# Optimization experiments

Measured on AMD Instinct MI355X. Metric: run time of the kernel, lower is better.

Reference implementation:

```python
import jax, jax.numpy as jnp
import numpy as np


def setup_inputs() -> dict:
    key = jax.random.key(0)
    ks = jax.random.split(key, 5)
    B, S, H = 64, 1024, 1024
    scale = 1.0 / np.sqrt(H)
    return {
        "decoder_hidden": jax.random.normal(ks[0], (B, H), jnp.float32),
        "encoder_outputs": jax.random.normal(ks[1], (B, S, H), jnp.float32),
        "W1": jax.random.normal(ks[2], (H, H), jnp.float32) * scale,
        "W2": jax.random.normal(ks[3], (H, H), jnp.float32) * scale,
        "v": jax.random.normal(ks[4], (H,), jnp.float32) * scale,
    }


def reference(decoder_hidden, encoder_outputs, W1, W2, v):
    # W1 @ decoder_hidden: [B, H] computed once, broadcast over src_len
    dh_proj = jnp.einsum("bh,oh->bo", decoder_hidden, W1)          # [B, H]
    enc_proj = jnp.einsum("bsh,oh->bso", encoder_outputs, W2)      # [B, S, H]
    energy = jnp.tanh(dh_proj[:, None, :] + enc_proj)              # [B, S, H]
    scores = jnp.einsum("bsh,h->bs", energy, v)                    # [B, S]
    attention_weights = jax.nn.softmax(scores, axis=-1)            # [B, S]
    context = jnp.einsum("bs,bsh->bh", attention_weights, encoder_outputs)
    return (context, attention_weights)
```

## Files before the change

kernel.cpp:

```cpp
#include <hip/hip_runtime.h>
#include <hip/hip_bf16.h>
#include <cmath>

#define Hdim 1024
#define Bdim 64
#define Sdim 1024

typedef __attribute__((ext_vector_type(4))) float f32x4;
typedef __attribute__((ext_vector_type(8))) short s16x8;
typedef __attribute__((ext_vector_type(4))) unsigned int u32x4;

static __device__ __forceinline__ unsigned short f2bf(float f) {
  unsigned int u = __builtin_bit_cast(unsigned int, f);
  unsigned int r = (u + 0x7fffu + ((u >> 16) & 1u)) >> 16;
  return (unsigned short)r;
}

static __device__ __forceinline__ float bf2f(unsigned short u) {
  return __builtin_bit_cast(float, (unsigned int)u << 16);
}

#define TANH_C 2.885390081777927f


static __device__ __forceinline__ void stage_rows64(const float* __restrict__ src,
                                                    unsigned short* As, int tid) {
  #pragma unroll 4
  for (int i = 0; i < 32; ++i) {
    int c = tid + i * 256;
    int row = c >> 7;
    int k8 = (c & 127) << 3;
    const float4* p = reinterpret_cast<const float4*>(src + row * Hdim + k8);
    float4 a = p[0];
    float4 b = p[1];
    union { unsigned short us[8]; u32x4 v; } pk;
    pk.us[0] = f2bf(a.x); pk.us[1] = f2bf(a.y); pk.us[2] = f2bf(a.z); pk.us[3] = f2bf(a.w);
    pk.us[4] = f2bf(b.x); pk.us[5] = f2bf(b.y); pk.us[6] = f2bf(b.z); pk.us[7] = f2bf(b.w);
    int idx = row * Hdim + (k8 ^ ((row & 7) << 3));
    *reinterpret_cast<u32x4*>(&As[idx]) = pk.v;
  }
}

static __device__ __forceinline__ s16x8 lda_full(const unsigned short* As, int row, int k) {
  int idx = row * Hdim + (k ^ ((row & 7) << 3));
  return *reinterpret_cast<const s16x8*>(&As[idx]);
}

static __device__ __forceinline__ s16x8 ldb_g(const unsigned short* __restrict__ Wb,
                                              const float* __restrict__ Wf,
                                              int use_bf, int o, int k) {
  if (use_bf) {
    return *reinterpret_cast<const s16x8*>(&Wb[o * Hdim + k]);
  } else {
    const float4* p = reinterpret_cast<const float4*>(Wf + o * Hdim + k);
    float4 a = p[0];
    float4 b = p[1];
    union { unsigned short us[8]; s16x8 v; } pk;
    pk.us[0] = f2bf(a.x); pk.us[1] = f2bf(a.y); pk.us[2] = f2bf(a.z); pk.us[3] = f2bf(a.w);
    pk.us[4] = f2bf(b.x); pk.us[5] = f2bf(b.y); pk.us[6] = f2bf(b.z); pk.us[7] = f2bf(b.w);
    return pk.v;
  }
}

__global__ void cast_bf16_kernel(const float* __restrict__ src,
                                 unsigned short* __restrict__ dst) {
  int i = blockIdx.x * 256 + threadIdx.x;
  const float4* p = reinterpret_cast<const float4*>(src) + i * 2;
  float4 a = p[0];
  float4 b = p[1];
  union { unsigned short us[8]; u32x4 v; } pk;
  pk.us[0] = f2bf(a.x); pk.us[1] = f2bf(a.y); pk.us[2] = f2bf(a.z); pk.us[3] = f2bf(a.w);
  pk.us[4] = f2bf(b.x); pk.us[5] = f2bf(b.y); pk.us[6] = f2bf(b.z); pk.us[7] = f2bf(b.w);
  *reinterpret_cast<u32x4*>(dst + i * 8) = pk.v;
}

__global__ __launch_bounds__(256, 1) void proj_kernel(
    const float* __restrict__ dh, const float* __restrict__ W1f,
    const unsigned short* __restrict__ W1b, float* __restrict__ out, int use_bf) {
  __shared__ unsigned short As[64 * Hdim];
  int tid = threadIdx.x;
  stage_rows64(dh, As, tid);
  __syncthreads();
  int w = tid >> 6, lane = tid & 63;
  int lo = lane & 15, hi = lane >> 4;
  int o = blockIdx.x * 16 + lo;
  f32x4 acc = {0.f, 0.f, 0.f, 0.f};
  for (int k0 = 0; k0 < Hdim; k0 += 32) {
    int k = k0 + hi * 8;
    s16x8 bfrag = ldb_g(W1b, W1f, use_bf, o, k);
    s16x8 afrag = lda_full(As, w * 16 + lo, k);
    acc = __builtin_amdgcn_mfma_f32_16x16x32_bf16(afrag, bfrag, acc, 0, 0, 0);
  }
  #pragma unroll
  for (int r = 0; r < 4; ++r)
    out[(w * 16 + hi * 4 + r) * Hdim + o] = acc[r];
}

#define SBM 128
#define SBN 128
#define SBK 64

__global__ __launch_bounds__(256, 3) void score_mfma_kernel(
    const unsigned short* __restrict__ encb,
    const unsigned short* __restrict__ W2b,
    const float* __restrict__ dhp, const float* __restrict__ v,
    float* __restrict__ scores) {
  __shared__ unsigned short As[2][SBM * SBK];
  __shared__ unsigned short Bs[2][SBN * SBK];
  __shared__ float ssum[SBM];
  int tid = threadIdx.x;
  int bid = blockIdx.x;
  int swz = (bid & 7) * 512 + (bid >> 3);
  int mp = swz >> 3;
  int np = swz & 7;
  int row0 = mp * SBM;
  int b = row0 >> 10;
  int w = tid >> 6, lane = tid & 63;
  int wr = w >> 1, wc = w & 1;
  int lo = lane & 15, hi = lane >> 4;

  if (tid < SBM) ssum[tid] = 0.f;

  const unsigned short* gA[4];
  const unsigned short* gB[4];
  #pragma unroll
  for (int i = 0; i < 4; ++i) {
    int d = i * 256 + tid;
    int row = d >> 3, c = d & 7;
    int gc = c ^ (row & 7);
    gA[i] = encb + (size_t)(row0 + row) * Hdim + gc * 8;
    gB[i] = W2b + (size_t)(np * SBN + row) * Hdim + gc * 8;
  }

  auto STAGE = [&](int buf) {
    #pragma unroll
    for (int i = 0; i < 4; ++i) {
      int dwv = i * 256 + w * 64;
      __builtin_amdgcn_global_load_lds(
          (const __attribute__((address_space(1))) unsigned int*)gA[i],
          (__attribute__((address_space(3))) unsigned int*)(&As[buf][dwv * 8]), 16, 0, 0);
      __builtin_amdgcn_global_load_lds(
          (const __attribute__((address_space(1))) unsigned int*)gB[i],
          (__attribute__((address_space(3))) unsigned int*)(&Bs[buf][dwv * 8]), 16, 0, 0);
      gA[i] += SBK;
      gB[i] += SBK;
    }
  };

  f32x4 acc[4][4] = {};

  STAGE(0);
  asm volatile("s_waitcnt vmcnt(0)" ::: "memory");
  __syncthreads();

  int cur = 0;
  for (int t = 0; t < 16; ++t) {
    if (t < 15) STAGE(cur ^ 1);

    const char* Ab = (const char*)As[cur];
    const char* Bb = (const char*)Bs[cur];
    #pragma unroll
    for (int ks = 0; ks < 2; ++ks) {
      int kb = (ks * 32 + hi * 8) * 2;
      s16x8 af[4], bf[4];
      #pragma unroll
      for (int m = 0; m < 4; ++m) {
        int row = wr * 64 + m * 16 + lo;
        af[m] = *reinterpret_cast<const s16x8*>(Ab + row * (SBK * 2) + (kb ^ ((row & 7) << 4)));
      }
      #pragma unroll
      for (int n = 0; n < 4; ++n) {
        int row = wc * 64 + n * 16 + lo;
        bf[n] = *reinterpret_cast<const s16x8*>(Bb + row * (SBK * 2) + (kb ^ ((row & 7) << 4)));
      }
      #pragma unroll
      for (int m = 0; m < 4; ++m)
        #pragma unroll
        for (int n = 0; n < 4; ++n)
          acc[m][n] = __builtin_amdgcn_mfma_f32_16x16x32_bf16(af[m], bf[n], acc[m][n], 0, 0, 0);
    }
    asm volatile("s_waitcnt vmcnt(0)" ::: "memory");
    __syncthreads();
    cur ^= 1;
  }

  float psum[4][4] = {};
  #pragma unroll
  for (int n = 0; n < 4; ++n) {
    int o = np * SBN + wc * 64 + n * 16 + lo;
    float dv = dhp[b * Hdim + o];
    float vv = v[o];
    float vv2 = 2.f * vv;
    #pragma unroll
    for (int m = 0; m < 4; ++m)
      #pragma unroll
      for (int r = 0; r < 4; ++r) {
        float x = acc[m][n][r] + dv;
        float e2 = __builtin_amdgcn_exp2f(x * TANH_C);
        float rc = __builtin_amdgcn_rcpf(1.f + e2);
        psum[m][r] += vv - vv2 * rc;
      }
  }
  #pragma unroll
  for (int mask = 1; mask < 16; mask <<= 1)
    #pragma unroll
    for (int m = 0; m < 4; ++m)
      #pragma unroll
      for (int r = 0; r < 4; ++r)
        psum[m][r] += __shfl_xor(psum[m][r], mask, 64);
  if (lo == 0) {
    #pragma unroll
    for (int m = 0; m < 4; ++m)
      #pragma unroll
      for (int r = 0; r < 4; ++r)
        atomicAdd(&ssum[wr * 64 + m * 16 + hi * 4 + r], psum[m][r]);
  }
  __syncthreads();
  if (tid < SBM) atomicAdd(&scores[row0 + tid], ssum[tid]);
}

#define BKt 64

__global__ __launch_bounds__(256, 3) void score_kernel(
    const float* __restrict__ enc, const float* __restrict__ W2f,
    const unsigned short* __restrict__ W2b, const float* __restrict__ dhp,
    const float* __restrict__ v, float* __restrict__ scores, int use_bf) {
  __shared__ unsigned short As[64 * BKt];
  int tid = threadIdx.x;
  int bid = blockIdx.x;
  int f = (bid & 7) * 512 + (bid >> 3);
  int rg = f >> 2;
  int oc = f & 3;
  int row0 = rg * 64;
  int b = row0 >> 10;
  int w = tid >> 6, lane = tid & 63;
  int lo = lane & 15, hi = lane >> 4;
  int n0 = oc * 256 + w * 64;

  const unsigned short* pB[4];
  const float* pBf[4];
  #pragma unroll
  for (int n = 0; n < 4; ++n) {
    int o = n0 + n * 16 + lo;
    pB[n]  = W2b + (size_t)o * Hdim + hi * 8;
    pBf[n] = W2f + (size_t)o * Hdim + hi * 8;
  }

  f32x4 acc[4][4] = {};

  for (int t = 0; t < 16; ++t) {
    int k0 = t * BKt;
    __syncthreads();
    #pragma unroll
    for (int cc = 0; cc < 2; ++cc) {
      int c = tid + cc * 256;
      int row = c >> 3;
      int j = c & 7;
      const float4* p = reinterpret_cast<const float4*>(
          enc + (size_t)(row0 + row) * Hdim + k0 + j * 8);
      float4 a = p[0];
      float4 bb = p[1];
      union { unsigned short us[8]; u32x4 v4; } pk;
      pk.us[0] = f2bf(a.x);  pk.us[1] = f2bf(a.y);  pk.us[2] = f2bf(a.z);  pk.us[3] = f2bf(a.w);
      pk.us[4] = f2bf(bb.x); pk.us[5] = f2bf(bb.y); pk.us[6] = f2bf(bb.z); pk.us[7] = f2bf(bb.w);
      int idx = row * BKt + ((j * 8) ^ ((row & 7) << 3));
      *reinterpret_cast<u32x4*>(&As[idx]) = pk.v4;
    }
    __syncthreads();

    #pragma unroll
    for (int ks = 0; ks < 2; ++ks) {
      s16x8 bfrag[4];
      #pragma unroll
      for (int n = 0; n < 4; ++n) {
        if (use_bf) {
          bfrag[n] = *reinterpret_cast<const s16x8*>(pB[n] + ks * 32);
        } else {
          const float4* p = reinterpret_cast<const float4*>(pBf[n] + ks * 32);
          float4 a = p[0];
          float4 bb = p[1];
          union { unsigned short us[8]; s16x8 v4; } pk;
          pk.us[0] = f2bf(a.x);  pk.us[1] = f2bf(a.y);  pk.us[2] = f2bf(a.z);  pk.us[3] = f2bf(a.w);
          pk.us[4] = f2bf(bb.x); pk.us[5] = f2bf(bb.y); pk.us[6] = f2bf(bb.z); pk.us[7] = f2bf(bb.w);
          bfrag[n] = pk.v4;
        }
      }
      #pragma unroll
      for (int m = 0; m < 4; ++m) {
        int kk = ks * 32 + hi * 8;
        s16x8 afrag = *reinterpret_cast<const s16x8*>(
            &As[(m * 16 + lo) * BKt + (kk ^ ((lo & 7) << 3))]);
        #pragma unroll
        for (int n = 0; n < 4; ++n)
          acc[m][n] = __builtin_amdgcn_mfma_f32_16x16x32_bf16(afrag, bfrag[n], acc[m][n], 0, 0, 0);
      }
    }
    #pragma unroll
    for (int n = 0; n < 4; ++n) { pB[n] += BKt; pBf[n] += BKt; }
  }

  float psum[4][4] = {};
  #pragma unroll
  for (int n = 0; n < 4; ++n) {
    int o = n0 + n * 16 + lo;
    float dv = dhp[b * Hdim + o];
    float vv = v[o];
    float vv2 = 2.f * vv;
    #pragma unroll
    for (int m = 0; m < 4; ++m)
      #pragma unroll
      for (int r = 0; r < 4; ++r) {
        float x = acc[m][n][r] + dv;
        float e2 = __builtin_amdgcn_exp2f(x * TANH_C);
        float rc = __builtin_amdgcn_rcpf(1.f + e2);
        psum[m][r] += vv - vv2 * rc;
      }
  }
  #pragma unroll
  for (int mask = 1; mask < 16; mask <<= 1)
    #pragma unroll
    for (int m = 0; m < 4; ++m)
      #pragma unroll
      for (int r = 0; r < 4; ++r)
        psum[m][r] += __shfl_xor(psum[m][r], mask, 64);
  if (lo == 0) {
    #pragma unroll
    for (int m = 0; m < 4; ++m)
      #pragma unroll
      for (int r = 0; r < 4; ++r)
        atomicAdd(&scores[row0 + m * 16 + hi * 4 + r], psum[m][r]);
  }
}

__global__ __launch_bounds__(256, 1) void softmax_kernel(float* __restrict__ attn) {
  __shared__ float redm[4];
  __shared__ float reds[4];
  int b = blockIdx.x, tid = threadIdx.x;
  float4 x = *reinterpret_cast<float4*>(attn + b * Sdim + tid * 4);
  float m = fmaxf(fmaxf(x.x, x.y), fmaxf(x.z, x.w));
  #pragma unroll
  for (int mask = 1; mask < 64; mask <<= 1) m = fmaxf(m, __shfl_xor(m, mask, 64));
  if ((tid & 63) == 0) redm[tid >> 6] = m;
  __syncthreads();
  m = fmaxf(fmaxf(redm[0], redm[1]), fmaxf(redm[2], redm[3]));
  float4 e;
  e.x = expf(x.x - m); e.y = expf(x.y - m); e.z = expf(x.z - m); e.w = expf(x.w - m);
  float s = e.x + e.y + e.z + e.w;
  #pragma unroll
  for (int mask = 1; mask < 64; mask <<= 1) s += __shfl_xor(s, mask, 64);
  if ((tid & 63) == 0) reds[tid >> 6] = s;
  __syncthreads();
  s = reds[0] + reds[1] + reds[2] + reds[3];
  float inv = 1.f / s;
  e.x *= inv; e.y *= inv; e.z *= inv; e.w *= inv;
  *reinterpret_cast<float4*>(attn + b * Sdim + tid * 4) = e;
}

__global__ __launch_bounds__(256, 1) void context_bf_kernel(
    const unsigned short* __restrict__ encb, const float* __restrict__ attn,
    float* __restrict__ ctx) {
  int b = blockIdx.x >> 4;
  int chunk = blockIdx.x & 15;
  int tid = threadIdx.x;
  int h0 = tid * 4;
  const unsigned short* ebase = encb + ((size_t)(b * Sdim + chunk * 64)) * Hdim + h0;
  const float* abase = attn + b * Sdim + chunk * 64;
  float4 acc = {0.f, 0.f, 0.f, 0.f};
  #pragma unroll 4
  for (int s = 0; s < 64; ++s) {
    float wgt = abase[s];
    ushort4 ev = *reinterpret_cast<const ushort4*>(ebase + (size_t)s * Hdim);
    acc.x += wgt * bf2f(ev.x);
    acc.y += wgt * bf2f(ev.y);
    acc.z += wgt * bf2f(ev.z);
    acc.w += wgt * bf2f(ev.w);
  }
  float* c = ctx + b * Hdim + h0;
  atomicAdd(c + 0, acc.x);
  atomicAdd(c + 1, acc.y);
  atomicAdd(c + 2, acc.z);
  atomicAdd(c + 3, acc.w);
}

__global__ __launch_bounds__(256, 1) void context_kernel(
    const float* __restrict__ enc, const float* __restrict__ attn,
    float* __restrict__ ctx) {
  int b = blockIdx.x >> 3;
  int chunk = blockIdx.x & 7;
  int tid = threadIdx.x;
  int h0 = tid * 4;
  const float* ebase = enc + ((size_t)(b * Sdim + chunk * 128)) * Hdim + h0;
  const float* abase = attn + b * Sdim + chunk * 128;
  float4 acc = {0.f, 0.f, 0.f, 0.f};
  #pragma unroll 4
  for (int s = 0; s < 128; ++s) {
    float wgt = abase[s];
    float4 ev = *reinterpret_cast<const float4*>(ebase + (size_t)s * Hdim);
    acc.x += wgt * ev.x; acc.y += wgt * ev.y; acc.z += wgt * ev.z; acc.w += wgt * ev.w;
  }
  float* c = ctx + b * Hdim + h0;
  atomicAdd(c + 0, acc.x);
  atomicAdd(c + 1, acc.y);
  atomicAdd(c + 2, acc.z);
  atomicAdd(c + 3, acc.w);
}

extern "C" void kernel_launch(void* const* d_in, const int* in_sizes, int n_in,
                              void* d_out, int out_size, void* d_ws, size_t ws_size,
                              hipStream_t stream) {
  const float* dh  = (const float*)d_in[0];
  const float* enc = (const float*)d_in[1];
  const float* W1  = (const float*)d_in[2];
  const float* W2  = (const float*)d_in[3];
  const float* v   = (const float*)d_in[4];
  float* out_ctx  = (float*)d_out;
  float* out_attn = out_ctx + Bdim * Hdim;

  int use_bf = (ws_size >= 4ull * 1024 * 1024) ? 1 : 0;
  int big_ws = (ws_size >= 133ull * 1024 * 1024) ? 1 : 0;
  unsigned short* W1b  = (unsigned short*)d_ws;
  unsigned short* W2b  = W1b + 1024 * 1024;
  unsigned short* encb = W2b + 1024 * 1024;

  if (use_bf) {
    cast_bf16_kernel<<<512, 256, 0, stream>>>(W1, W1b);
    cast_bf16_kernel<<<512, 256, 0, stream>>>(W2, W2b);
  }
  if (big_ws) {
    cast_bf16_kernel<<<32768, 256, 0, stream>>>(enc, encb);
  }

  proj_kernel<<<64, 256, 0, stream>>>(dh, W1, W1b, out_ctx, use_bf);

  hipMemsetAsync(out_attn, 0, (size_t)Bdim * Sdim * sizeof(float), stream);
  if (big_ws) {
    score_mfma_kernel<<<4096, 256, 0, stream>>>(encb, W2b, out_ctx, v, out_attn);
  } else {
    score_kernel<<<4096, 256, 0, stream>>>(enc, W2, W2b, out_ctx, v, out_attn, use_bf);
  }

  softmax_kernel<<<Bdim, 256, 0, stream>>>(out_attn);

  hipMemsetAsync(out_ctx, 0, (size_t)Bdim * Hdim * sizeof(float), stream);
  if (big_ws) {
    context_bf_kernel<<<1024, 256, 0, stream>>>(encb, out_attn, out_ctx);
  } else {
    context_kernel<<<512, 256, 0, stream>>>(enc, out_attn, out_ctx);
  }
}
```

Baseline: 325.0 us.

## Load W2 fragments directly from global into registers, bypassing LDS

```diff
diff --git a/kernel.cpp b/kernel.cpp
--- a/kernel.cpp
+++ b/kernel.cpp
@@ -106,7 +106,6 @@
     const float* __restrict__ dhp, const float* __restrict__ v,
     float* __restrict__ scores) {
   __shared__ unsigned short As[2][SBM * SBK];
-  __shared__ unsigned short Bs[2][SBN * SBK];
   __shared__ float ssum[SBM];
   int tid = threadIdx.x;
   int bid = blockIdx.x;
@@ -122,14 +121,12 @@
   if (tid < SBM) ssum[tid] = 0.f;
 
   const unsigned short* gA[4];
-  const unsigned short* gB[4];
   #pragma unroll
   for (int i = 0; i < 4; ++i) {
     int d = i * 256 + tid;
     int row = d >> 3, c = d & 7;
     int gc = c ^ (row & 7);
     gA[i] = encb + (size_t)(row0 + row) * Hdim + gc * 8;
-    gB[i] = W2b + (size_t)(np * SBN + row) * Hdim + gc * 8;
   }
 
   auto STAGE = [&](int buf) {
@@ -139,48 +136,65 @@
       __builtin_amdgcn_global_load_lds(
           (const __attribute__((address_space(1))) unsigned int*)gA[i],
           (__attribute__((address_space(3))) unsigned int*)(&As[buf][dwv * 8]), 16, 0, 0);
-      __builtin_amdgcn_global_load_lds(
-          (const __attribute__((address_space(1))) unsigned int*)gB[i],
-          (__attribute__((address_space(3))) unsigned int*)(&Bs[buf][dwv * 8]), 16, 0, 0);
       gA[i] += SBK;
-      gB[i] += SBK;
     }
   };
 
-  f32x4 acc[4][4] = {};
-
+  const unsigned short* pB[4];
+  #pragma unroll
+  for (int n = 0; n < 4; ++n) {
+    int o = np * SBN + wc * 64 + n * 16 + lo;
+    pB[n] = W2b + (size_t)o * Hdim + hi * 8;
+  }
+
+  s16x8 bfc[2][4], bfn[2][4];
+
+  #pragma unroll
+  for (int ks = 0; ks < 2; ++ks)
+    #pragma unroll
+    for (int n = 0; n < 4; ++n)
+      bfc[ks][n] = *reinterpret_cast<const s16x8*>(pB[n] + ks * 32);
   STAGE(0);
   asm volatile("s_waitcnt vmcnt(0)" ::: "memory");
   __syncthreads();
 
+  f32x4 acc[4][4] = {};
   int cur = 0;
   for (int t = 0; t < 16; ++t) {
-    if (t < 15) STAGE(cur ^ 1);
+    if (t < 15) {
+      #pragma unroll
+      for (int ks = 0; ks < 2; ++ks)
+        #pragma unroll
+        for (int n = 0; n < 4; ++n)
+          bfn[ks][n] = *reinterpret_cast<const s16x8*>(pB[n] + (t + 1) * SBK + ks * 32);
+      STAGE(cur ^ 1);
+    }
 
     const char* Ab = (const char*)As[cur];
-    const char* Bb = (const char*)Bs[cur];
     #pragma unroll
     for (int ks = 0; ks < 2; ++ks) {
       int kb = (ks * 32 + hi * 8) * 2;
-      s16x8 af[4], bf[4];
+      s16x8 af[4];
       #pragma unroll
       for (int m = 0; m < 4; ++m) {
         int row = wr * 64 + m * 16 + lo;
         af[m] = *reinterpret_cast<const s16x8*>(Ab + row * (SBK * 2) + (kb ^ ((row & 7) << 4)));
       }
       #pragma unroll
-      for (int n = 0; n < 4; ++n) {
-        int row = wc * 64 + n * 16 + lo;
-        bf[n] = *reinterpret_cast<const s16x8*>(Bb + row * (SBK * 2) + (kb ^ ((row & 7) << 4)));
-      }
-      #pragma unroll
       for (int m = 0; m < 4; ++m)
         #pragma unroll
         for (int n = 0; n < 4; ++n)
-          acc[m][n] = __builtin_amdgcn_mfma_f32_16x16x32_bf16(af[m], bf[n], acc[m][n], 0, 0, 0);
+          acc[m][n] = __builtin_amdgcn_mfma_f32_16x16x32_bf16(af[m], bfc[ks][n], acc[m][n], 0, 0, 0);
     }
     asm volatile("s_waitcnt vmcnt(0)" ::: "memory");
     __syncthreads();
+    if (t < 15) {
+      #pragma unroll
+      for (int ks = 0; ks < 2; ++ks)
+        #pragma unroll
+        for (int n = 0; n < 4; ++n)
+          bfc[ks][n] = bfn[ks][n];
+    }
     cur ^= 1;
   }
 
```

New measurement: 398.0 us. 1.22x slower.

## Enlarge score GEMM tile to 256 rows with 512 threads, single-buffer LDS

Applied to the files above, without the earlier changes.

```diff
diff --git a/kernel.cpp b/kernel.cpp
--- a/kernel.cpp
+++ b/kernel.cpp
@@ -65,12 +65,12 @@
 __global__ void cast_bf16_kernel(const float* __restrict__ src,
                                  unsigned short* __restrict__ dst) {
   int i = blockIdx.x * 256 + threadIdx.x;
-  const float4* p = reinterpret_cast<const float4*>(src) + i * 2;
-  float4 a = p[0];
-  float4 b = p[1];
+  const f32x4* p = reinterpret_cast<const f32x4*>(src) + i * 2;
+  f32x4 a = __builtin_nontemporal_load(p);
+  f32x4 b = __builtin_nontemporal_load(p + 1);
   union { unsigned short us[8]; u32x4 v; } pk;
-  pk.us[0] = f2bf(a.x); pk.us[1] = f2bf(a.y); pk.us[2] = f2bf(a.z); pk.us[3] = f2bf(a.w);
-  pk.us[4] = f2bf(b.x); pk.us[5] = f2bf(b.y); pk.us[6] = f2bf(b.z); pk.us[7] = f2bf(b.w);
+  pk.us[0] = f2bf(a[0]); pk.us[1] = f2bf(a[1]); pk.us[2] = f2bf(a[2]); pk.us[3] = f2bf(a[3]);
+  pk.us[4] = f2bf(b[0]); pk.us[5] = f2bf(b[1]); pk.us[6] = f2bf(b[2]); pk.us[7] = f2bf(b[3]);
   *reinterpret_cast<u32x4*>(dst + i * 8) = pk.v;
 }
 
@@ -96,21 +96,20 @@
     out[(w * 16 + hi * 4 + r) * Hdim + o] = acc[r];
 }
 
-#define SBM 128
+#define SBM 256
 #define SBN 128
 #define SBK 64
 
-__global__ __launch_bounds__(256, 3) void score_mfma_kernel(
+__global__ __launch_bounds__(512, 4) void score_mfma_kernel(
     const unsigned short* __restrict__ encb,
     const unsigned short* __restrict__ W2b,
     const float* __restrict__ dhp, const float* __restrict__ v,
     float* __restrict__ scores) {
-  __shared__ unsigned short As[2][SBM * SBK];
-  __shared__ unsigned short Bs[2][SBN * SBK];
-  __shared__ float ssum[SBM];
+  __shared__ unsigned short As[SBM * SBK];
+  __shared__ unsigned short Bs[SBN * SBK];
   int tid = threadIdx.x;
   int bid = blockIdx.x;
-  int swz = (bid & 7) * 512 + (bid >> 3);
+  int swz = (bid & 7) * 256 + (bid >> 3);
   int mp = swz >> 3;
   int np = swz & 7;
   int row0 = mp * SBM;
@@ -118,47 +117,34 @@
   int w = tid >> 6, lane = tid & 63;
   int wr = w >> 1, wc = w & 1;
   int lo = lane & 15, hi = lane >> 4;
-
-  if (tid < SBM) ssum[tid] = 0.f;
-
-  const unsigned short* gA[4];
-  const unsigned short* gB[4];
-  #pragma unroll
-  for (int i = 0; i < 4; ++i) {
-    int d = i * 256 + tid;
-    int row = d >> 3, c = d & 7;
-    int gc = c ^ (row & 7);
-    gA[i] = encb + (size_t)(row0 + row) * Hdim + gc * 8;
-    gB[i] = W2b + (size_t)(np * SBN + row) * Hdim + gc * 8;
-  }
-
-  auto STAGE = [&](int buf) {
-    #pragma unroll
-    for (int i = 0; i < 4; ++i) {
-      int dwv = i * 256 + w * 64;
+  int xorv = (lo & 7) << 4;
+
+  int srow = tid >> 3;
+  int gc = (tid & 7) ^ (srow & 7);
+  const unsigned short* gA0 = encb + (size_t)(row0 + srow) * Hdim + gc * 8;
+  const unsigned short* gB0 = W2b + (size_t)(np * SBN + srow) * Hdim + gc * 8;
+
+  f32x4 acc[4][4] = {};
+
+  for (int t = 0; t < 16; ++t) {
+    __syncthreads();
+    #pragma unroll
+    for (int g = 0; g < 4; ++g) {
       __builtin_amdgcn_global_load_lds(
-          (const __attribute__((address_space(1))) unsigned int*)gA[i],
-          (__attribute__((address_space(3))) unsigned int*)(&As[buf][dwv * 8]), 16, 0, 0);
+          (const __attribute__((address_space(1))) unsigned int*)(gA0 + (size_t)g * 64 * Hdim + t * SBK),
+          (__attribute__((address_space(3))) unsigned int*)(&As[(g * 512 + w * 64) * 8]), 16, 0, 0);
+    }
+    #pragma unroll
+    for (int g = 0; g < 2; ++g) {
       __builtin_amdgcn_global_load_lds(
-          (const __attribute__((address_space(1))) unsigned int*)gB[i],
-          (__attribute__((address_space(3))) unsigned int*)(&Bs[buf][dwv * 8]), 16, 0, 0);
-      gA[i] += SBK;
-      gB[i] += SBK;
+          (const __attribute__((address_space(1))) unsigned int*)(gB0 + (size_t)g * 64 * Hdim + t * SBK),
+          (__attribute__((address_space(3))) unsigned int*)(&Bs[(g * 512 + w * 64) * 8]), 16, 0, 0);
     }
-  };
-
-  f32x4 acc[4][4] = {};
-
-  STAGE(0);
-  asm volatile("s_waitcnt vmcnt(0)" ::: "memory");
-  __syncthreads();
-
-  int cur = 0;
-  for (int t = 0; t < 16; ++t) {
-    if (t < 15) STAGE(cur ^ 1);
-
-    const char* Ab = (const char*)As[cur];
-    const char* Bb = (const char*)Bs[cur];
+    asm volatile("s_waitcnt vmcnt(0)" ::: "memory");
+    __syncthreads();
+
+    const char* Ab = (const char*)As;
+    const char* Bb = (const char*)Bs;
     #pragma unroll
     for (int ks = 0; ks < 2; ++ks) {
       int kb = (ks * 32 + hi * 8) * 2;
@@ -166,12 +152,12 @@
       #pragma unroll
       for (int m = 0; m < 4; ++m) {
         int row = wr * 64 + m * 16 + lo;
-        af[m] = *reinterpret_cast<const s16x8*>(Ab + row * (SBK * 2) + (kb ^ ((row & 7) << 4)));
+        af[m] = *reinterpret_cast<const s16x8*>(Ab + row * 128 + (kb ^ xorv));
       }
       #pragma unroll
       for (int n = 0; n < 4; ++n) {
         int row = wc * 64 + n * 16 + lo;
-        bf[n] = *reinterpret_cast<const s16x8*>(Bb + row * (SBK * 2) + (kb ^ ((row & 7) << 4)));
+        bf[n] = *reinterpret_cast<const s16x8*>(Bb + row * 128 + (kb ^ xorv));
       }
       #pragma unroll
       for (int m = 0; m < 4; ++m)
@@ -179,9 +165,6 @@
         for (int n = 0; n < 4; ++n)
           acc[m][n] = __builtin_amdgcn_mfma_f32_16x16x32_bf16(af[m], bf[n], acc[m][n], 0, 0, 0);
     }
-    asm volatile("s_waitcnt vmcnt(0)" ::: "memory");
-    __syncthreads();
-    cur ^= 1;
   }
 
   float psum[4][4] = {};
@@ -213,10 +196,8 @@
     for (int m = 0; m < 4; ++m)
       #pragma unroll
       for (int r = 0; r < 4; ++r)
-        atomicAdd(&ssum[wr * 64 + m * 16 + hi * 4 + r], psum[m][r]);
-  }
-  __syncthreads();
-  if (tid < SBM) atomicAdd(&scores[row0 + tid], ssum[tid]);
+        atomicAdd(&scores[row0 + wr * 64 + m * 16 + hi * 4 + r], psum[m][r]);
+  }
 }
 
 #define BKt 64
@@ -434,7 +415,7 @@
 
   hipMemsetAsync(out_attn, 0, (size_t)Bdim * Sdim * sizeof(float), stream);
   if (big_ws) {
-    score_mfma_kernel<<<4096, 256, 0, stream>>>(encb, W2b, out_ctx, v, out_attn);
+    score_mfma_kernel<<<2048, 512, 0, stream>>>(encb, W2b, out_ctx, v, out_attn);
   } else {
     score_kernel<<<4096, 256, 0, stream>>>(enc, W2, W2b, out_ctx, v, out_attn, use_bf);
   }
```

Result: faster. 303.2 us (-6.7%).
